# Kernel optimization log

Measured on AMD Instinct MI355X. Metric: run time of the kernel, lower is better.

Reference implementation:

```python
import jax, jax.numpy as jnp
import numpy as np

B, OBS, H, M, L1, T, A = 16384, 376, 512, 8, 3, 50, 17  # L1 = num_layers - 1
LOG_SQRT_2PI = 0.5 * np.log(2.0 * np.pi).astype(np.float32)


def setup_inputs() -> dict:
    key = jax.random.key(0)
    ks = jax.random.split(key, 16)
    s = lambda fan: 1.0 / np.sqrt(fan).astype(np.float32)
    return {
        "x": jax.random.normal(ks[0], (B, OBS), jnp.float32),
        "task_idx": jax.random.randint(ks[1], (B,), 0, T, jnp.int64),
        "enc_W1": jax.random.normal(ks[2], (OBS, H), jnp.float32) * s(OBS),
        "enc_b1": jnp.zeros((H,), jnp.float32),
        "enc_W2": jax.random.normal(ks[3], (H, H), jnp.float32) * s(H),
        "enc_b2": jnp.zeros((H,), jnp.float32),
        "task_emb": jax.random.normal(ks[4], (T, H), jnp.float32),
        "a_rW": jax.random.normal(ks[5], (L1, H, M * M), jnp.float32) * s(H),
        "a_rb": jnp.zeros((L1, M * M), jnp.float32),
        "c_rW": jax.random.normal(ks[6], (L1, H, M * M), jnp.float32) * s(H),
        "c_rb": jnp.zeros((L1, M * M), jnp.float32),
        "a_W": jax.random.normal(ks[7], (L1, M, H, H), jnp.float32) * s(H),
        "a_b": jnp.zeros((L1, M, H), jnp.float32),
        "a_Wf": jax.random.normal(ks[8], (M, H, A), jnp.float32) * 0.01,
        "a_bf": jnp.zeros((M, A), jnp.float32),
        "c_W": jax.random.normal(ks[9], (L1, M, H, H), jnp.float32) * s(H),
        "c_b": jnp.zeros((L1, M, H), jnp.float32),
        "c_Wf": jax.random.normal(ks[10], (M, H, 1), jnp.float32) * s(H),
        "c_bf": jnp.zeros((M, 1), jnp.float32),
        "actor_logstd": jnp.zeros((1, A), jnp.float32),
    }


def _routing(context, rW, rb):
    # context: [B,H]; rW: [L1,H,M*M] -> list of [B,M,M] softmax routing probs
    rel = jax.nn.relu(context)
    probs = []
    for l in range(L1):
        logits = (rel @ rW[l] + rb[l]).reshape(-1, M, M)
        probs.append(jax.nn.softmax(logits, axis=2))
    return probs


def _base(f_s, probs, W, b, Wf, bf):
    # f_s: [B,H]; W: [L1,M,H,H]; Wf: [M,H,out]
    g = jnp.broadcast_to(f_s[:, None, :], (f_s.shape[0], M, H))  # [B,M,H]
    for l in range(L1):
        outs = jax.nn.relu(jnp.einsum("bmh,mhk->bmk", g, W[l]) + b[l])  # [B,M,H]
        g = jnp.einsum("bij,bjh->bih", probs[l], outs)  # soft combine
    final = jnp.einsum("bmh,mhk->bmk", g, Wf) + bf  # [B,M,out]
    return final.sum(axis=1)


def reference(x, task_idx, enc_W1, enc_b1, enc_W2, enc_b2, task_emb,
              a_rW, a_rb, c_rW, c_rb, a_W, a_b, a_Wf, a_bf,
              c_W, c_b, c_Wf, c_bf, actor_logstd):
    f_s = jnp.tanh(jnp.tanh(x @ enc_W1 + enc_b1) @ enc_W2 + enc_b2)  # [B,H]
    h_z = task_emb[task_idx]  # [B,H]
    context = f_s * h_z

    value = _base(f_s, _routing(context, c_rW, c_rb), c_W, c_b, c_Wf, c_bf)  # [B,1]
    mean = _base(f_s, _routing(context, a_rW, a_rb), a_W, a_b, a_Wf, a_bf)   # [B,A]

    # deterministic action (sample=False): action = mean
    logstd = jnp.broadcast_to(actor_logstd, mean.shape)
    log_prob = (-logstd - LOG_SQRT_2PI).sum(axis=1)          # N.log_prob(mean).sum(1)
    entropy = (0.5 + LOG_SQRT_2PI + logstd).sum(axis=1)
    # concat (action, log_prob, entropy, value) -> [B, A+3]
    return jnp.concatenate([mean, log_prob[:, None], entropy[:, None], value], axis=1)
```

## Files before the change

kernel.cpp:

```cpp
#include <hip/hip_runtime.h>
#include <hip/hip_bf16.h>

typedef float f32x4 __attribute__((ext_vector_type(4)));
typedef float f32x2 __attribute__((ext_vector_type(2)));
typedef int   i32x4 __attribute__((ext_vector_type(4)));
typedef int   i32x8 __attribute__((ext_vector_type(8)));

#define LOG_SQRT_2PI 0.91893853320467274f

static constexpr int BSZ  = 16384;
static constexpr int OBSN = 376;
static constexpr int HD   = 512;
static constexpr int NACT = 17;

__device__ __forceinline__ unsigned char f2fp8(float v) {
  return (unsigned char)(__builtin_amdgcn_cvt_pk_fp8_f32(v, v, 0, false) & 0xFF);
}

__device__ __forceinline__ void xcd_map(int id, int gx, int gy, int& bx, int& by, int& bz) {
  int p = id & 7, l = id >> 3;
  bx = l % gx;
  int g = (l / gx) * 8 + p;
  by = g % gy;
  bz = g / gy;
}


__global__ void k_cvt_pad8(const float* __restrict__ src, unsigned char* __restrict__ dst) {
  long i = (long)blockIdx.x * 256 + threadIdx.x;
  if (i >= (long)BSZ * HD) return;
  long r = i >> 9;
  int  c = (int)(i & 511);
  dst[i] = f2fp8(c < OBSN ? src[r * OBSN + c] : 0.f);
}

__global__ void k_packT8(const float* __restrict__ src, unsigned char* __restrict__ dst,
                         int K, int N, int Kpad, long sstride, long dstride, float scale) {
  __shared__ float t[32][33];
  src += (long)blockIdx.z * sstride;
  dst += (long)blockIdx.z * dstride;
  int k0 = blockIdx.y * 32, n0 = blockIdx.x * 32;
#pragma unroll
  for (int ii = 0; ii < 4; ++ii) {
    int i = ii * 8 + threadIdx.y;
    int k = k0 + i, n = n0 + threadIdx.x;
    t[i][threadIdx.x] = (k < K && n < N) ? src[(long)k * N + n] : 0.f;
  }
  __syncthreads();
#pragma unroll
  for (int ii = 0; ii < 4; ++ii) {
    int i = ii * 8 + threadIdx.y;
    int n = n0 + i, k = k0 + threadIdx.x;
    if (n < N && k < Kpad) dst[(long)n * Kpad + k] = f2fp8(scale * t[threadIdx.x][i]);
  }
}

__global__ void k_packw8(const float* __restrict__ aW, const float* __restrict__ cW,
                         unsigned char* __restrict__ dst) {
  __shared__ float t[32][33];
  const int z = blockIdx.z;
  const float* src = (z < 24) ? aW + (long)z * 262144 : cW + (long)(z - 24) * 262144;
  unsigned char* d = dst + (long)z * 262144;
  int k0 = blockIdx.y * 32, n0 = blockIdx.x * 32;
#pragma unroll
  for (int ii = 0; ii < 4; ++ii) {
    int i = ii * 8 + threadIdx.y;
    t[i][threadIdx.x] = src[(long)(k0 + i) * 512 + n0 + threadIdx.x];
  }
  __syncthreads();
#pragma unroll
  for (int ii = 0; ii < 4; ++ii) {
    int i = ii * 8 + threadIdx.y;
    d[(long)(n0 + i) * 512 + k0 + threadIdx.x] = f2fp8(16.f * t[threadIdx.x][i]);
  }
}

__global__ void k_packwf8(const float* __restrict__ aWf, const float* __restrict__ cWf,
                          unsigned char* __restrict__ dsta, unsigned char* __restrict__ dstc) {
  int i = blockIdx.x * 256 + threadIdx.x;
  int n = i >> 12, k = i & 4095;
  dsta[i] = (n < NACT) ? f2fp8(64.f * aWf[(long)k * NACT + n]) : (unsigned char)0;
  dstc[i] = (n < 1)    ? f2fp8(64.f * cWf[k])                  : (unsigned char)0;
}

__global__ void k_pack_rb(const float* __restrict__ a_rb, const float* __restrict__ c_rb,
                          float* __restrict__ rb) {
  int i = threadIdx.x;
  rb[i] = (i < 192) ? a_rb[i] : c_rb[i - 192];
}

__global__ void k_sum_bf(const float* __restrict__ a_bf, const float* __restrict__ c_bf,
                         float* __restrict__ sa, float* __restrict__ sc) {
  int a = threadIdx.x;
  if (a < NACT) { float s = 0.f; for (int m = 0; m < 8; ++m) s += a_bf[m * NACT + a]; sa[a] = s; }
  if (a == 0)   { float s = 0.f; for (int m = 0; m < 8; ++m) s += c_bf[m];            sc[0] = s; }
}

template <int OP>
__global__ __launch_bounds__(256, 4)
void k_gemm8(const unsigned char* __restrict__ A, const unsigned char* __restrict__ Bt,
             void* __restrict__ Cv, const float* __restrict__ bias,
             int N, int K, int lda, int ldc, int gx, int gy,
             int a_zoff, int b_zoff, int c_zoff, int bias_zoff,
             const int* __restrict__ tidx, const float* __restrict__ temb,
             unsigned char* __restrict__ out2) {
  __shared__ alignas(16) unsigned char sA[128 * 128];
  __shared__ alignas(16) unsigned char sB[128 * 128];
  int bx, by, z;
  xcd_map(blockIdx.x, gx, gy, bx, by, z);
  A  += (long)z * a_zoff;
  Bt += (long)z * b_zoff;
  const int tid  = threadIdx.x;
  const int wave = tid >> 6, lane = tid & 63;
  const int wr = (wave >> 1) * 64, wc = (wave & 1) * 64;
  const int row0 = by * 128, col0 = bx * 128;
  const int lcol = lane & 15, quad = lane >> 4;
  const int sw7 = lcol & 7;
  const int c0 = ((2 * quad)     ^ sw7) * 16;
  const int c1 = ((2 * quad + 1) ^ sw7) * 16;
  const int raA0 = (wr + lcol) * 128 + c0, raA1 = (wr + lcol) * 128 + c1;
  const int rbB0 = (wc + lcol) * 128 + c0, rbB1 = (wc + lcol) * 128 + c1;
  int aOff[4], bOff[4];
#pragma unroll
  for (int i = 0; i < 4; ++i) {
    int u = i * 256 + tid;
    int r = u >> 3, gc = (u & 7) ^ (r & 7);
    aOff[i] = (row0 + r) * lda + gc * 16;
    bOff[i] = (col0 + r) * K + gc * 16;
  }

  f32x4 acc[4][4] = {};

  for (int kt = 0; kt < K; kt += 128) {
#pragma unroll
    for (int i = 0; i < 4; ++i)
      __builtin_amdgcn_global_load_lds(
          (const __attribute__((address_space(1))) void*)(A + aOff[i] + kt),
          (__attribute__((address_space(3))) void*)&sA[i * 4096 + tid * 16], 16, 0, 0);
#pragma unroll
    for (int i = 0; i < 4; ++i)
      __builtin_amdgcn_global_load_lds(
          (const __attribute__((address_space(1))) void*)(Bt + bOff[i] + kt),
          (__attribute__((address_space(3))) void*)&sB[i * 4096 + tid * 16], 16, 0, 0);
    __syncthreads();
    i32x8 bv[4];
#pragma unroll
    for (int ni = 0; ni < 4; ++ni) {
      i32x4 blo = *(const i32x4*)&sB[rbB0 + ni * 2048];
      i32x4 bhi = *(const i32x4*)&sB[rbB1 + ni * 2048];
      bv[ni] = (i32x8){blo[0], blo[1], blo[2], blo[3], bhi[0], bhi[1], bhi[2], bhi[3]};
    }
#pragma unroll
    for (int mi = 0; mi < 4; ++mi) {
      i32x4 alo = *(const i32x4*)&sA[raA0 + mi * 2048];
      i32x4 ahi = *(const i32x4*)&sA[raA1 + mi * 2048];
      i32x8 af = (i32x8){alo[0], alo[1], alo[2], alo[3], ahi[0], ahi[1], ahi[2], ahi[3]};
#pragma unroll
      for (int ni = 0; ni < 4; ++ni)
        acc[mi][ni] = __builtin_amdgcn_mfma_scale_f32_16x16x128_f8f6f4(
            bv[ni], af, acc[mi][ni], 0, 0, 0, 0x7F, 0, 0x7F);
    }
    __syncthreads();
  }

#pragma unroll
  for (int ni = 0; ni < 4; ++ni) {
    int colb = col0 + wc + ni * 16 + quad * 4;
    if (colb >= N) continue;
    float4 bw = *(const float4*)&bias[(long)z * bias_zoff + colb];
#pragma unroll
    for (int mi = 0; mi < 4; ++mi) {
      int rowg = row0 + wr + mi * 16 + lcol;
      float v0 = acc[mi][ni][0] * 0.0625f + bw.x;
      float v1 = acc[mi][ni][1] * 0.0625f + bw.y;
      float v2 = acc[mi][ni][2] * 0.0625f + bw.z;
      float v3 = acc[mi][ni][3] * 0.0625f + bw.w;
      long idx = (long)rowg * ldc + (long)z * c_zoff + colb;
      if (OP == 0) {
        unsigned d = __builtin_amdgcn_cvt_pk_fp8_f32(fmaxf(v0, 0.f), fmaxf(v1, 0.f), 0, false);
        d = __builtin_amdgcn_cvt_pk_fp8_f32(fmaxf(v2, 0.f), fmaxf(v3, 0.f), d, true);
        *(unsigned*)&((unsigned char*)Cv)[idx] = d;
      } else if (OP == 1) {
        float t0 = tanhf(v0), t1 = tanhf(v1), t2 = tanhf(v2), t3 = tanhf(v3);
        unsigned d = __builtin_amdgcn_cvt_pk_fp8_f32(t0, t1, 0, false);
        d = __builtin_amdgcn_cvt_pk_fp8_f32(t2, t3, d, true);
        *(unsigned*)&((unsigned char*)Cv)[idx] = d;
      } else if (OP == 5) {
        float t0 = tanhf(v0), t1 = tanhf(v1), t2 = tanhf(v2), t3 = tanhf(v3);
        unsigned d = __builtin_amdgcn_cvt_pk_fp8_f32(t0, t1, 0, false);
        d = __builtin_amdgcn_cvt_pk_fp8_f32(t2, t3, d, true);
        *(unsigned*)&((unsigned char*)Cv)[idx] = d;
        int tk = tidx[rowg];
        float4 te = *(const float4*)&temb[(long)tk * HD + colb];
        unsigned e = __builtin_amdgcn_cvt_pk_fp8_f32(fmaxf(t0 * te.x, 0.f), fmaxf(t1 * te.y, 0.f), 0, false);
        e = __builtin_amdgcn_cvt_pk_fp8_f32(fmaxf(t2 * te.z, 0.f), fmaxf(t3 * te.w, 0.f), e, true);
        *(unsigned*)&out2[idx] = e;
      } else if (OP == 4) {
        float mx = fmaxf(fmaxf(v0, v1), fmaxf(v2, v3));
        mx = fmaxf(mx, __shfl_xor(mx, 16));
        float e0 = __expf(v0 - mx), e1 = __expf(v1 - mx), e2 = __expf(v2 - mx), e3 = __expf(v3 - mx);
        float s = e0 + e1 + e2 + e3;
        s += __shfl_xor(s, 16);
        float inv = 1.f / s;
        *(float4*)&((float*)Cv)[idx] = make_float4(e0 * inv, e1 * inv, e2 * inv, e3 * inv);
      }
    }
  }
}

__global__ __launch_bounds__(256)
void k_combine8(const unsigned char* __restrict__ outs, const float* __restrict__ probs,
                unsigned char* __restrict__ g, int poff) {
  __shared__ float P[4][64];
  const int w = threadIdx.x >> 6, l = threadIdx.x & 63;
  const long b = (long)blockIdx.x * 4 + w;
  P[w][l] = probs[b * 384 + poff + l];
  __syncthreads();
  const unsigned char* ob = outs + b * 4096 + l * 8;
  float o[8][8];
#pragma unroll
  for (int j = 0; j < 8; ++j) {
    uint2 v = *(const uint2*)(ob + j * 512);
    f32x2 p01 = __builtin_amdgcn_cvt_pk_f32_fp8(v.x, false);
    f32x2 p23 = __builtin_amdgcn_cvt_pk_f32_fp8(v.x, true);
    f32x2 p45 = __builtin_amdgcn_cvt_pk_f32_fp8(v.y, false);
    f32x2 p67 = __builtin_amdgcn_cvt_pk_f32_fp8(v.y, true);
    o[j][0] = p01.x; o[j][1] = p01.y; o[j][2] = p23.x; o[j][3] = p23.y;
    o[j][4] = p45.x; o[j][5] = p45.y; o[j][6] = p67.x; o[j][7] = p67.y;
  }
  unsigned char* gb = g + b * 4096 + l * 8;
#pragma unroll
  for (int i = 0; i < 8; ++i) {
    float a[8] = {};
#pragma unroll
    for (int j = 0; j < 8; ++j) {
      float pw = P[w][i * 8 + j];
#pragma unroll
      for (int c = 0; c < 8; ++c) a[c] += pw * o[j][c];
    }
    unsigned int lo = __builtin_amdgcn_cvt_pk_fp8_f32(a[0], a[1], 0, false);
    lo = __builtin_amdgcn_cvt_pk_fp8_f32(a[2], a[3], lo, true);
    unsigned int hi = __builtin_amdgcn_cvt_pk_fp8_f32(a[4], a[5], 0, false);
    hi = __builtin_amdgcn_cvt_pk_fp8_f32(a[6], a[7], hi, true);
    *(uint2*)(gb + i * 512) = make_uint2(lo, hi);
  }
}

template <int NOUT>
__global__ __launch_bounds__(256)
void k_head8(const unsigned char* __restrict__ A, const unsigned char* __restrict__ Bt,
             const float* __restrict__ bsum, float* __restrict__ out, int ooff) {
  __shared__ alignas(16) unsigned char sA[64 * 64];
  __shared__ alignas(16) unsigned char sB[32 * 64];
  const int tid = threadIdx.x;
  const int wave = tid >> 6, lane = tid & 63;
  const int row0 = blockIdx.x * 64;
  const int lcol = lane & 15, quad = lane >> 4;
  const int sw = (lcol >> 1) & 3;
  const int co0 = (((quad >> 1)    ) ^ sw) * 16 + (quad & 1) * 8;
  const int co1 = (((quad >> 1) + 2) ^ sw) * 16 + (quad & 1) * 8;
  f32x4 acc[2] = {};

  for (int kt = 0; kt < 4096; kt += 64) {
    {
      int r = tid >> 2, gc = (tid & 3) ^ ((tid >> 3) & 3);
      const unsigned char* ga = A + (long)(row0 + r) * 4096 + kt + gc * 16;
      __builtin_amdgcn_global_load_lds((const __attribute__((address_space(1))) void*)ga,
                                       (__attribute__((address_space(3))) void*)&sA[tid * 16], 16, 0, 0);
    }
    if (tid < 128) {
      int r = tid >> 2, gc = (tid & 3) ^ ((tid >> 3) & 3);
      const unsigned char* gb = Bt + (long)r * 4096 + kt + gc * 16;
      __builtin_amdgcn_global_load_lds((const __attribute__((address_space(1))) void*)gb,
                                       (__attribute__((address_space(3))) void*)&sB[tid * 16], 16, 0, 0);
    }
    __syncthreads();
    long af[2], bv[2][2];
    int ra = (wave * 16 + lcol) * 64;
    af[0] = *(const long*)&sA[ra + co0];
    af[1] = *(const long*)&sA[ra + co1];
#pragma unroll
    for (int ni = 0; ni < 2; ++ni) {
      int rb = (ni * 16 + lcol) * 64;
      bv[0][ni] = *(const long*)&sB[rb + co0];
      bv[1][ni] = *(const long*)&sB[rb + co1];
    }
#pragma unroll
    for (int kk = 0; kk < 2; ++kk)
#pragma unroll
      for (int ni = 0; ni < 2; ++ni)
        acc[ni] = __builtin_amdgcn_mfma_f32_16x16x32_fp8_fp8(af[kk], bv[kk][ni], acc[ni], 0, 0, 0);
    __syncthreads();
  }

#pragma unroll
  for (int ni = 0; ni < 2; ++ni) {
    int col = ni * 16 + lcol;
    if (col >= NOUT) continue;
#pragma unroll
    for (int r = 0; r < 4; ++r) {
      int row = row0 + wave * 16 + quad * 4 + r;
      out[(long)row * 20 + ooff + col] = acc[ni][r] * 0.015625f + bsum[col];
    }
  }
}

__global__ void k_logstd(const float* __restrict__ ls, float* __restrict__ out) {
  float lp = 0.f, ent = 0.f;
#pragma unroll
  for (int a = 0; a < NACT; ++a) {
    float v = ls[a];
    lp  += -v - LOG_SQRT_2PI;
    ent += 0.5f + LOG_SQRT_2PI + v;
  }
  long b = (long)blockIdx.x * 256 + threadIdx.x;
  if (b < BSZ) { out[b * 20 + 17] = lp; out[b * 20 + 18] = ent; }
}


extern "C" void kernel_launch(void* const* d_in, const int* in_sizes, int n_in,
                              void* d_out, int out_size, void* d_ws, size_t ws_size,
                              hipStream_t stream) {
  const float* x        = (const float*)d_in[0];
  const int*   task_idx = (const int*)d_in[1];
  const float* enc_W1   = (const float*)d_in[2];
  const float* enc_b1   = (const float*)d_in[3];
  const float* enc_W2   = (const float*)d_in[4];
  const float* enc_b2   = (const float*)d_in[5];
  const float* task_emb = (const float*)d_in[6];
  const float* a_rW     = (const float*)d_in[7];
  const float* a_rb     = (const float*)d_in[8];
  const float* c_rW     = (const float*)d_in[9];
  const float* c_rb     = (const float*)d_in[10];
  const float* a_W      = (const float*)d_in[11];
  const float* a_b      = (const float*)d_in[12];
  const float* a_Wf     = (const float*)d_in[13];
  const float* a_bf     = (const float*)d_in[14];
  const float* c_W      = (const float*)d_in[15];
  const float* c_b      = (const float*)d_in[16];
  const float* c_Wf     = (const float*)d_in[17];
  const float* c_bf     = (const float*)d_in[18];
  const float* logstd   = (const float*)d_in[19];
  float* out = (float*)d_out;

  char* ws = (char*)d_ws;
  size_t off = 0;
  auto carve = [&](size_t bytes) {
    char* p = ws + off;
    off += (bytes + 255) & ~(size_t)255;
    return p;
  };
  unsigned char* W8 = (unsigned char*)carve((size_t)48 * 262144);
  unsigned char* W1T8 = (unsigned char*)carve((size_t)512 * 512);
  unsigned char* W2T8 = (unsigned char*)carve((size_t)512 * 512);
  unsigned char* rWT8 = (unsigned char*)carve((size_t)384 * 512);
  float* rball = (float*)carve(384 * 4);
  unsigned char* WfaT8 = (unsigned char*)carve((size_t)32 * 4096);
  unsigned char* WfcT8 = (unsigned char*)carve((size_t)32 * 4096);
  float* bfa   = (float*)carve(128 * 4);
  float* bfc   = (float*)carve(128 * 4);
  unsigned char* fs8 = (unsigned char*)carve((size_t)BSZ * HD);
  float* lgt   = (float*)carve((size_t)BSZ * 384 * 4);

  size_t remain = (ws_size > off) ? (ws_size - off) : 0;
  int Bc = 4096;
  for (int cand = BSZ; cand > 4096; cand >>= 1)
    if ((size_t)2 * cand * 4096 <= remain) { Bc = cand; break; }
  size_t half = (size_t)Bc * 4096;
  unsigned char* bufA8 = (unsigned char*)carve(half);
  unsigned char* bufB8 = (unsigned char*)carve(half);
  unsigned char* x8   = bufA8;
  unsigned char* h18  = bufB8;
  unsigned char* rel8 = bufA8;

  dim3 tb(32, 8);

  k_cvt_pad8<<<(int)(((long)BSZ * HD + 255) / 256), 256, 0, stream>>>(x, x8);
  k_packT8<<<dim3(16, 16, 1), tb, 0, stream>>>(enc_W1, W1T8, OBSN, 512, 512, 0, 0, 16.f);
  k_packT8<<<dim3(16, 16, 1), tb, 0, stream>>>(enc_W2, W2T8, 512, 512, 512, 0, 0, 16.f);
  k_packT8<<<dim3(2, 16, 3),  tb, 0, stream>>>(a_rW, rWT8,             512, 64, 512, 512 * 64, 64 * 512, 16.f);
  k_packT8<<<dim3(2, 16, 3),  tb, 0, stream>>>(c_rW, rWT8 + 192 * 512, 512, 64, 512, 512 * 64, 64 * 512, 16.f);
  k_packw8<<<dim3(16, 16, 48), tb, 0, stream>>>(a_W, c_W, W8);
  k_packwf8<<<512, 256, 0, stream>>>(a_Wf, c_Wf, WfaT8, WfcT8);
  k_pack_rb<<<1, 384, 0, stream>>>(a_rb, c_rb, rball);
  k_sum_bf<<<1, 32, 0, stream>>>(a_bf, c_bf, bfa, bfc);

  const int GY = BSZ / 128;
  k_gemm8<1><<<4 * GY, 256, 0, stream>>>(x8, W1T8, h18, enc_b1, 512, 512, 512, 512,
                                         4, GY, 0, 0, 0, 0, nullptr, nullptr, nullptr);
  k_gemm8<5><<<4 * GY, 256, 0, stream>>>(h18, W2T8, fs8, enc_b2, 512, 512, 512, 512,
                                         4, GY, 0, 0, 0, 0, task_idx, task_emb, rel8);
  k_gemm8<4><<<3 * GY, 256, 0, stream>>>(rel8, rWT8, lgt, rball, 384, 512, 512, 384,
                                         3, GY, 0, 0, 0, 0, nullptr, nullptr, nullptr);

  const size_t wz8 = (size_t)8 * 262144;
  const unsigned char* W8a = W8;
  const unsigned char* W8c = W8 + (size_t)24 * 262144;
  for (int c0 = 0; c0 < BSZ; c0 += Bc) {
    const unsigned char* fs_c = fs8 + (long)c0 * 512;
    const float* pr_c  = lgt + (long)c0 * 384;
    float*       out_c = out + (long)c0 * 20;
    const int gy = Bc / 128;

    k_gemm8<0><<<32 * gy, 256, 0, stream>>>(fs_c, W8c, bufA8, c_b, 4096, 512, 512, 4096,
                                            32, gy, 0, 0, 0, 0, nullptr, nullptr, nullptr);
    k_combine8<<<Bc / 4, 256, 0, stream>>>(bufA8, pr_c, bufB8, 192 + 0);
    k_gemm8<0><<<4 * gy * 8, 256, 0, stream>>>(bufB8, W8c + 1 * wz8, bufA8, c_b + 4096,
                                               512, 512, 4096, 4096, 4, gy, 512, 262144, 512, 512,
                                               nullptr, nullptr, nullptr);
    k_combine8<<<Bc / 4, 256, 0, stream>>>(bufA8, pr_c, bufB8, 192 + 64);
    k_gemm8<0><<<4 * gy * 8, 256, 0, stream>>>(bufB8, W8c + 2 * wz8, bufA8, c_b + 8192,
                                               512, 512, 4096, 4096, 4, gy, 512, 262144, 512, 512,
                                               nullptr, nullptr, nullptr);
    k_combine8<<<Bc / 4, 256, 0, stream>>>(bufA8, pr_c, bufB8, 192 + 128);
    k_head8<1><<<Bc / 64, 256, 0, stream>>>(bufB8, WfcT8, bfc, out_c, 19);

    k_gemm8<0><<<32 * gy, 256, 0, stream>>>(fs_c, W8a, bufA8, a_b, 4096, 512, 512, 4096,
                                            32, gy, 0, 0, 0, 0, nullptr, nullptr, nullptr);
    k_combine8<<<Bc / 4, 256, 0, stream>>>(bufA8, pr_c, bufB8, 0);
    k_gemm8<0><<<4 * gy * 8, 256, 0, stream>>>(bufB8, W8a + 1 * wz8, bufA8, a_b + 4096,
                                               512, 512, 4096, 4096, 4, gy, 512, 262144, 512, 512,
                                               nullptr, nullptr, nullptr);
    k_combine8<<<Bc / 4, 256, 0, stream>>>(bufA8, pr_c, bufB8, 64);
    k_gemm8<0><<<4 * gy * 8, 256, 0, stream>>>(bufB8, W8a + 2 * wz8, bufA8, a_b + 8192,
                                               512, 512, 4096, 4096, 4, gy, 512, 262144, 512, 512,
                                               nullptr, nullptr, nullptr);
    k_combine8<<<Bc / 4, 256, 0, stream>>>(bufA8, pr_c, bufB8, 128);
    k_head8<NACT><<<Bc / 64, 256, 0, stream>>>(bufB8, WfaT8, bfa, out_c, 0);
  }

  k_logstd<<<BSZ / 256, 256, 0, stream>>>(logstd, out);
}
```

Baseline: 796.8 us.

## Merge actor and critic branch GEMMs and stage FP8 epilogue stores through LDS

The actor and critic expert weights and biases are repacked per layer and interleaved, so each layer's GEMM and combine runs once over both networks (8192 columns) instead of once per network. This halves the number of launches and gives each launch a larger grid, at the cost of double-sized intermediate buffers and possibly a smaller batch chunk. The OP==0 epilogue now writes ReLU'd FP8 tiles into swizzled LDS and then issues coalesced 16-byte global stores, replacing scattered 4-byte stores.

```diff
diff --git a/kernel.cpp b/kernel.cpp
--- a/kernel.cpp
+++ b/kernel.cpp
@@ -59,7 +59,8 @@
                          unsigned char* __restrict__ dst) {
   __shared__ float t[32][33];
   const int z = blockIdx.z;
-  const float* src = (z < 24) ? aW + (long)z * 262144 : cW + (long)(z - 24) * 262144;
+  const int layer = z >> 4, zz = z & 15, net = zz >> 3, m = zz & 7;
+  const float* src = (net ? aW : cW) + (long)(layer * 8 + m) * 262144;
   unsigned char* d = dst + (long)z * 262144;
   int k0 = blockIdx.y * 32, n0 = blockIdx.x * 32;
 #pragma unroll
@@ -73,6 +74,15 @@
     int i = ii * 8 + threadIdx.y;
     d[(long)(n0 + i) * 512 + k0 + threadIdx.x] = f2fp8(16.f * t[threadIdx.x][i]);
   }
+}
+
+__global__ void k_pack_lb(const float* __restrict__ a_b, const float* __restrict__ c_b,
+                          float* __restrict__ lb) {
+  int i = blockIdx.x * 256 + threadIdx.x;
+  if (i >= 24576) return;
+  int layer = i >> 13, zz = (i >> 9) & 15, n = i & 511;
+  int net = zz >> 3, m = zz & 7;
+  lb[i] = (net ? a_b : c_b)[(layer * 8 + m) * 512 + n];
 }
 
 __global__ void k_packwf8(const float* __restrict__ aWf, const float* __restrict__ cWf,
@@ -163,6 +173,37 @@
     __syncthreads();
   }
 
+  if (OP == 0) {
+#pragma unroll
+    for (int ni = 0; ni < 4; ++ni) {
+      int colb = col0 + wc + ni * 16 + quad * 4;
+      float4 bw = *(const float4*)&bias[(long)z * bias_zoff + colb];
+      int chunk = (wc >> 4) + ni;
+#pragma unroll
+      for (int mi = 0; mi < 4; ++mi) {
+        int rowl = wr + mi * 16 + lcol;
+        float v0 = fmaxf(acc[mi][ni][0] * 0.0625f + bw.x, 0.f);
+        float v1 = fmaxf(acc[mi][ni][1] * 0.0625f + bw.y, 0.f);
+        float v2 = fmaxf(acc[mi][ni][2] * 0.0625f + bw.z, 0.f);
+        float v3 = fmaxf(acc[mi][ni][3] * 0.0625f + bw.w, 0.f);
+        unsigned d = __builtin_amdgcn_cvt_pk_fp8_f32(v0, v1, 0, false);
+        d = __builtin_amdgcn_cvt_pk_fp8_f32(v2, v3, d, true);
+        *(unsigned*)&sA[rowl * 128 + ((chunk ^ (rowl & 7)) << 4) + quad * 4] = d;
+      }
+    }
+    __syncthreads();
+#pragma unroll
+    for (int i2 = 0; i2 < 4; ++i2) {
+      int u = i2 * 256 + tid;
+      int r = u >> 3, p = u & 7;
+      i32x4 v = *(const i32x4*)&sA[r * 128 + p * 16];
+      int chl = p ^ (r & 7);
+      long idx = (long)(row0 + r) * ldc + (long)z * c_zoff + col0 + chl * 16;
+      *(i32x4*)&((unsigned char*)Cv)[idx] = v;
+    }
+    return;
+  }
+
 #pragma unroll
   for (int ni = 0; ni < 4; ++ni) {
     int colb = col0 + wc + ni * 16 + quad * 4;
@@ -176,11 +217,7 @@
       float v2 = acc[mi][ni][2] * 0.0625f + bw.z;
       float v3 = acc[mi][ni][3] * 0.0625f + bw.w;
       long idx = (long)rowg * ldc + (long)z * c_zoff + colb;
-      if (OP == 0) {
-        unsigned d = __builtin_amdgcn_cvt_pk_fp8_f32(fmaxf(v0, 0.f), fmaxf(v1, 0.f), 0, false);
-        d = __builtin_amdgcn_cvt_pk_fp8_f32(fmaxf(v2, 0.f), fmaxf(v3, 0.f), d, true);
-        *(unsigned*)&((unsigned char*)Cv)[idx] = d;
-      } else if (OP == 1) {
+      if (OP == 1) {
         float t0 = tanhf(v0), t1 = tanhf(v1), t2 = tanhf(v2), t3 = tanhf(v3);
         unsigned d = __builtin_amdgcn_cvt_pk_fp8_f32(t0, t1, 0, false);
         d = __builtin_amdgcn_cvt_pk_fp8_f32(t2, t3, d, true);
@@ -210,13 +247,14 @@
 
 __global__ __launch_bounds__(256)
 void k_combine8(const unsigned char* __restrict__ outs, const float* __restrict__ probs,
-                unsigned char* __restrict__ g, int poff) {
+                unsigned char* __restrict__ g, int poffC, int poffA) {
   __shared__ float P[4][64];
   const int w = threadIdx.x >> 6, l = threadIdx.x & 63;
-  const long b = (long)blockIdx.x * 4 + w;
-  P[w][l] = probs[b * 384 + poff + l];
+  const int net = blockIdx.x & 1;
+  const long b = (long)(blockIdx.x >> 1) * 4 + w;
+  P[w][l] = probs[b * 384 + (net ? poffA : poffC) + l];
   __syncthreads();
-  const unsigned char* ob = outs + b * 4096 + l * 8;
+  const unsigned char* ob = outs + b * 8192 + net * 4096 + l * 8;
   float o[8][8];
 #pragma unroll
   for (int j = 0; j < 8; ++j) {
@@ -228,7 +266,7 @@
     o[j][0] = p01.x; o[j][1] = p01.y; o[j][2] = p23.x; o[j][3] = p23.y;
     o[j][4] = p45.x; o[j][5] = p45.y; o[j][6] = p67.x; o[j][7] = p67.y;
   }
-  unsigned char* gb = g + b * 4096 + l * 8;
+  unsigned char* gb = g + b * 8192 + net * 4096 + l * 8;
 #pragma unroll
   for (int i = 0; i < 8; ++i) {
     float a[8] = {};
@@ -249,7 +287,7 @@
 template <int NOUT>
 __global__ __launch_bounds__(256)
 void k_head8(const unsigned char* __restrict__ A, const unsigned char* __restrict__ Bt,
-             const float* __restrict__ bsum, float* __restrict__ out, int ooff) {
+             const float* __restrict__ bsum, float* __restrict__ out, int lda, int ooff) {
   __shared__ alignas(16) unsigned char sA[64 * 64];
   __shared__ alignas(16) unsigned char sB[32 * 64];
   const int tid = threadIdx.x;
@@ -264,7 +302,7 @@
   for (int kt = 0; kt < 4096; kt += 64) {
     {
       int r = tid >> 2, gc = (tid & 3) ^ ((tid >> 3) & 3);
-      const unsigned char* ga = A + (long)(row0 + r) * 4096 + kt + gc * 16;
+      const unsigned char* ga = A + (long)(row0 + r) * lda + kt + gc * 16;
       __builtin_amdgcn_global_load_lds((const __attribute__((address_space(1))) void*)ga,
                                        (__attribute__((address_space(3))) void*)&sA[tid * 16], 16, 0, 0);
     }
@@ -355,6 +393,7 @@
   unsigned char* W2T8 = (unsigned char*)carve((size_t)512 * 512);
   unsigned char* rWT8 = (unsigned char*)carve((size_t)384 * 512);
   float* rball = (float*)carve(384 * 4);
+  float* lb    = (float*)carve(3 * 16 * 512 * 4);
   unsigned char* WfaT8 = (unsigned char*)carve((size_t)32 * 4096);
   unsigned char* WfcT8 = (unsigned char*)carve((size_t)32 * 4096);
   float* bfa   = (float*)carve(128 * 4);
@@ -363,10 +402,10 @@
   float* lgt   = (float*)carve((size_t)BSZ * 384 * 4);
 
   size_t remain = (ws_size > off) ? (ws_size - off) : 0;
-  int Bc = 4096;
-  for (int cand = BSZ; cand > 4096; cand >>= 1)
-    if ((size_t)2 * cand * 4096 <= remain) { Bc = cand; break; }
-  size_t half = (size_t)Bc * 4096;
+  int Bc = 2048;
+  for (int cand = BSZ; cand > 2048; cand >>= 1)
+    if ((size_t)2 * cand * 8192 <= remain) { Bc = cand; break; }
+  size_t half = (size_t)Bc * 8192;
   unsigned char* bufA8 = (unsigned char*)carve(half);
   unsigned char* bufB8 = (unsigned char*)carve(half);
   unsigned char* x8   = bufA8;
@@ -381,6 +420,7 @@
   k_packT8<<<dim3(2, 16, 3),  tb, 0, stream>>>(a_rW, rWT8,             512, 64, 512, 512 * 64, 64 * 512, 16.f);
   k_packT8<<<dim3(2, 16, 3),  tb, 0, stream>>>(c_rW, rWT8 + 192 * 512, 512, 64, 512, 512 * 64, 64 * 512, 16.f);
   k_packw8<<<dim3(16, 16, 48), tb, 0, stream>>>(a_W, c_W, W8);
+  k_pack_lb<<<96, 256, 0, stream>>>(a_b, c_b, lb);
   k_packwf8<<<512, 256, 0, stream>>>(a_Wf, c_Wf, WfaT8, WfcT8);
   k_pack_rb<<<1, 384, 0, stream>>>(a_rb, c_rb, rball);
   k_sum_bf<<<1, 32, 0, stream>>>(a_bf, c_bf, bfa, bfc);
@@ -393,40 +433,26 @@
   k_gemm8<4><<<3 * GY, 256, 0, stream>>>(rel8, rWT8, lgt, rball, 384, 512, 512, 384,
                                          3, GY, 0, 0, 0, 0, nullptr, nullptr, nullptr);
 
-  const size_t wz8 = (size_t)8 * 262144;
-  const unsigned char* W8a = W8;
-  const unsigned char* W8c = W8 + (size_t)24 * 262144;
+  const size_t wlz = (size_t)16 * 262144;
   for (int c0 = 0; c0 < BSZ; c0 += Bc) {
     const unsigned char* fs_c = fs8 + (long)c0 * 512;
     const float* pr_c  = lgt + (long)c0 * 384;
     float*       out_c = out + (long)c0 * 20;
     const int gy = Bc / 128;
 
-    k_gemm8<0><<<32 * gy, 256, 0, stream>>>(fs_c, W8c, bufA8, c_b, 4096, 512, 512, 4096,
-                                            32, gy, 0, 0, 0, 0, nullptr, nullptr, nullptr);
-    k_combine8<<<Bc / 4, 256, 0, stream>>>(bufA8, pr_c, bufB8, 192 + 0);
-    k_gemm8<0><<<4 * gy * 8, 256, 0, stream>>>(bufB8, W8c + 1 * wz8, bufA8, c_b + 4096,
-                                               512, 512, 4096, 4096, 4, gy, 512, 262144, 512, 512,
-                                               nullptr, nullptr, nullptr);
-    k_combine8<<<Bc / 4, 256, 0, stream>>>(bufA8, pr_c, bufB8, 192 + 64);
-    k_gemm8<0><<<4 * gy * 8, 256, 0, stream>>>(bufB8, W8c + 2 * wz8, bufA8, c_b + 8192,
-                                               512, 512, 4096, 4096, 4, gy, 512, 262144, 512, 512,
-                                               nullptr, nullptr, nullptr);
-    k_combine8<<<Bc / 4, 256, 0, stream>>>(bufA8, pr_c, bufB8, 192 + 128);
-    k_head8<1><<<Bc / 64, 256, 0, stream>>>(bufB8, WfcT8, bfc, out_c, 19);
-
-    k_gemm8<0><<<32 * gy, 256, 0, stream>>>(fs_c, W8a, bufA8, a_b, 4096, 512, 512, 4096,
-                                            32, gy, 0, 0, 0, 0, nullptr, nullptr, nullptr);
-    k_combine8<<<Bc / 4, 256, 0, stream>>>(bufA8, pr_c, bufB8, 0);
-    k_gemm8<0><<<4 * gy * 8, 256, 0, stream>>>(bufB8, W8a + 1 * wz8, bufA8, a_b + 4096,
-                                               512, 512, 4096, 4096, 4, gy, 512, 262144, 512, 512,
-                                               nullptr, nullptr, nullptr);
-    k_combine8<<<Bc / 4, 256, 0, stream>>>(bufA8, pr_c, bufB8, 64);
-    k_gemm8<0><<<4 * gy * 8, 256, 0, stream>>>(bufB8, W8a + 2 * wz8, bufA8, a_b + 8192,
-                                               512, 512, 4096, 4096, 4, gy, 512, 262144, 512, 512,
-                                               nullptr, nullptr, nullptr);
-    k_combine8<<<Bc / 4, 256, 0, stream>>>(bufA8, pr_c, bufB8, 128);
-    k_head8<NACT><<<Bc / 64, 256, 0, stream>>>(bufB8, WfaT8, bfa, out_c, 0);
+    k_gemm8<0><<<64 * gy, 256, 0, stream>>>(fs_c, W8, bufA8, lb, 8192, 512, 512, 8192,
+                                            64, gy, 0, 0, 0, 0, nullptr, nullptr, nullptr);
+    k_combine8<<<Bc / 2, 256, 0, stream>>>(bufA8, pr_c, bufB8, 192 + 0, 0);
+    k_gemm8<0><<<64 * gy, 256, 0, stream>>>(bufB8, W8 + wlz, bufA8, lb + 8192,
+                                            512, 512, 8192, 8192, 4, gy, 512, 262144, 512, 512,
+                                            nullptr, nullptr, nullptr);
+    k_combine8<<<Bc / 2, 256, 0, stream>>>(bufA8, pr_c, bufB8, 192 + 64, 64);
+    k_gemm8<0><<<64 * gy, 256, 0, stream>>>(bufB8, W8 + 2 * wlz, bufA8, lb + 16384,
+                                            512, 512, 8192, 8192, 4, gy, 512, 262144, 512, 512,
+                                            nullptr, nullptr, nullptr);
+    k_combine8<<<Bc / 2, 256, 0, stream>>>(bufA8, pr_c, bufB8, 192 + 128, 128);
+    k_head8<1><<<Bc / 64, 256, 0, stream>>>(bufB8, WfcT8, bfc, out_c, 8192, 19);
+    k_head8<NACT><<<Bc / 64, 256, 0, stream>>>(bufB8 + 4096, WfaT8, bfa, out_c, 8192, 0);
   }
 
   k_logstd<<<BSZ / 256, 256, 0, stream>>>(logstd, out);
```

After: 768.3 us. 3.6% less time.
